# Optimization experiments

Measured on AMD Instinct MI355X. Metric: run time of the kernel, lower is better.

Reference implementation:

```python
import jax, jax.numpy as jnp
import numpy as np

EPS = 1e-8  # torch cosine_similarity default eps


def setup_inputs() -> dict:
    key = jax.random.key(0)
    x = jax.random.normal(key, (256, 200, 1024), dtype=jnp.float32)
    return {"x": x}


def reference(x):
    # x: [B, c, l]
    # Cosine-similarity Gram matrix, fused: dot(i,j) / max(||x_i||*||x_j||, eps)
    norms = jnp.linalg.norm(x, axis=-1)                      # [B, c]
    dots = jnp.einsum('bil,bjl->bij', x, x)                  # [B, c, c]
    sim = dots / jnp.maximum(norms[:, :, None] * norms[:, None, :], EPS)
    atten = jax.nn.softmax(sim, axis=-1)                     # [B, c, c]
    out = jnp.einsum('bij,bjl->bil', atten, x) + x           # bmm + residual
    return out
```

## Files before the change

kernel.cpp:

```cpp
#include <hip/hip_runtime.h>
#include <math.h>


typedef unsigned int uint32;
typedef __attribute__((ext_vector_type(8))) short bf16x8;
typedef __attribute__((ext_vector_type(4))) float f32x4;

#define CC 200
#define LL 1024
#define EPSV 1e-8f
#define PLSTR 116
#define XASTR 36
#define XBSTR 132

__device__ __forceinline__ uint32 bfb(float f) {
  uint32 u = __float_as_uint(f);
  u += 0x7fffu + ((u >> 16) & 1u);
  return u >> 16;
}

__global__ __launch_bounds__(512, 1)
void spe_attn_kernel(const float* __restrict__ x, float* __restrict__ out) {
  const int tid  = threadIdx.x;
  const int lane = tid & 63;
  const int w    = tid >> 6;
  const int lm   = lane & 15;
  const int lg   = lane >> 4;
  const int bidx = blockIdx.x;
  const float* xb = x + (size_t)bidx * (CC * LL);
  float* ob       = out + (size_t)bidx * (CC * LL);

  __shared__ uint32 LDS[39312];
  uint32* pl    = LDS;
  uint32* xa0   = LDS + 24128;
  uint32* xa1   = LDS + 31616;
  uint32* xbuf  = LDS + 24128;
  float*  norms = (float*)(LDS + 39104);

  const bool two = (w < 5);
  const int rb0 = w;
  const int rb1 = two ? (w + 8) : w;

  const f32x4 fz = {0.f, 0.f, 0.f, 0.f};
  f32x4 acc[2][13];
  #pragma unroll
  for (int i = 0; i < 2; ++i)
    #pragma unroll
    for (int j = 0; j < 13; ++j) acc[i][j] = fz;

  if (tid < 288) { xa0[7200 + tid] = 0u; xa1[7200 + tid] = 0u; }

  float4 vst[7];
  #pragma unroll
  for (int i = 0; i < 7; ++i) {
    int idx = tid + i * 512;
    if (idx < 3200) {
      int row = idx >> 4, c4 = idx & 15;
      vst[i] = *(const float4*)(xb + row * LL + c4 * 4);
    }
  }
  #pragma unroll
  for (int i = 0; i < 7; ++i) {
    int idx = tid + i * 512;
    if (idx < 3200) {
      int row = idx >> 4, c4 = idx & 15;
      uint2 wv;
      wv.x = bfb(vst[i].x) | (bfb(vst[i].y) << 16);
      wv.y = bfb(vst[i].z) | (bfb(vst[i].w) << 16);
      *(uint2*)&xa0[row * XASTR + c4 * 2] = wv;
    }
  }

  for (int s = 0; s < 16; ++s) {
    __syncthreads();
    if (s + 1 < 16) {
      #pragma unroll
      for (int i = 0; i < 7; ++i) {
        int idx = tid + i * 512;
        if (idx < 3200) {
          int row = idx >> 4, c4 = idx & 15;
          vst[i] = *(const float4*)(xb + row * LL + (s + 1) * 64 + c4 * 4);
        }
      }
    }
    const uint32* cur = (s & 1) ? xa1 : xa0;
    #pragma unroll
    for (int ks = 0; ks < 2; ++ks) {
      bf16x8 a0 = *(const bf16x8*)&cur[(rb0 * 16 + lm) * XASTR + ks * 16 + lg * 4];
      bf16x8 a1 = a0;
      if (two) a1 = *(const bf16x8*)&cur[(rb1 * 16 + lm) * XASTR + ks * 16 + lg * 4];
      #pragma unroll
      for (int ct = 0; ct < 13; ++ct) {
        bf16x8 bf = *(const bf16x8*)&cur[(ct * 16 + lm) * XASTR + ks * 16 + lg * 4];
        acc[0][ct] = __builtin_amdgcn_mfma_f32_16x16x32_bf16(a0, bf, acc[0][ct], 0, 0, 0);
        if (two)
          acc[1][ct] = __builtin_amdgcn_mfma_f32_16x16x32_bf16(a1, bf, acc[1][ct], 0, 0, 0);
      }
    }
    if (s + 1 < 16) {
      uint32* nxt = (s & 1) ? xa0 : xa1;
      #pragma unroll
      for (int i = 0; i < 7; ++i) {
        int idx = tid + i * 512;
        if (idx < 3200) {
          int row = idx >> 4, c4 = idx & 15;
          uint2 wv;
          wv.x = bfb(vst[i].x) | (bfb(vst[i].y) << 16);
          wv.y = bfb(vst[i].z) | (bfb(vst[i].w) << 16);
          *(uint2*)&nxt[row * XASTR + c4 * 2] = wv;
        }
      }
    }
  }

  #pragma unroll
  for (int rbi = 0; rbi < 2; ++rbi) {
    if (rbi == 0 || two) {
      int rb = rbi ? rb1 : rb0;
      #pragma unroll
      for (int ct = 0; ct < 13; ++ct) {
        if (ct == rb) {
          #pragma unroll
          for (int r = 0; r < 4; ++r) {
            int ri = lg * 4 + r;
            if (lm == ri) norms[rb * 16 + ri] = sqrtf(acc[rbi][ct][r]);
          }
        }
      }
    }
  }
  __syncthreads();

  float cn[13];
  #pragma unroll
  for (int ct = 0; ct < 13; ++ct) cn[ct] = norms[ct * 16 + lm];

  #pragma unroll
  for (int rbi = 0; rbi < 2; ++rbi) {
    if (rbi == 0 || two) {
      int rb = rbi ? rb1 : rb0;
      #pragma unroll
      for (int r = 0; r < 4; ++r) {
        int grow = rb * 16 + lg * 4 + r;
        float rn = norms[grow];
        float sv[13];
        float m = -INFINITY;
        #pragma unroll
        for (int ct = 0; ct < 13; ++ct) {
          int gc = ct * 16 + lm;
          float sval = acc[rbi][ct][r] / fmaxf(rn * cn[ct], EPSV);
          sval = (gc < CC) ? sval : -INFINITY;
          sv[ct] = sval;
          m = fmaxf(m, sval);
        }
        #pragma unroll
        for (int off = 1; off < 16; off <<= 1) m = fmaxf(m, __shfl_xor(m, off));
        float sum = 0.f;
        #pragma unroll
        for (int ct = 0; ct < 13; ++ct) {
          float e = __expf(sv[ct] - m);
          sv[ct] = e;
          sum += e;
        }
        #pragma unroll
        for (int off = 1; off < 16; off <<= 1) sum += __shfl_xor(sum, off);
        float inv = 1.0f / sum;
        #pragma unroll
        for (int ct = 0; ct < 13; ++ct) {
          int gc = ct * 16 + lm;
          float p = sv[ct] * inv + ((gc == grow) ? 1.0f : 0.0f);
          uint32 pb = bfb(p);
          uint32 qb = (uint32)__shfl_xor((int)pb, 1);
          if (!(lane & 1)) pl[grow * PLSTR + ct * 8 + (lm >> 1)] = pb | (qb << 16);
        }
      }
      for (int i = lane; i < 256; i += 64) {
        int rr = i >> 4, c = i & 15;
        if (c < 12) pl[(rb * 16 + rr) * PLSTR + 100 + c] = 0u;
      }
    }
  }

  bf16x8 pa[2][7];
  #pragma unroll
  for (int ks = 0; ks < 7; ++ks) {
    pa[0][ks] = *(const bf16x8*)&pl[(rb0 * 16 + lm) * PLSTR + ks * 16 + lg * 4];
    if (two)
      pa[1][ks] = *(const bf16x8*)&pl[(rb1 * 16 + lm) * PLSTR + ks * 16 + lg * 4];
  }

  float pva[14], pvb[14];
  #pragma unroll
  for (int p = 0; p < 14; ++p) {
    int kp = p * 8 + w;
    int r0 = kp * 2, r1 = r0 + 1;
    pva[p] = (r0 < CC) ? xb[r0 * LL + lane] : 0.f;
    pvb[p] = (r1 < CC) ? xb[r1 * LL + lane] : 0.f;
  }

  for (int nc = 0; nc < 16; ++nc) {
    const int n0 = nc * 64;
    __syncthreads();
    #pragma unroll
    for (int p = 0; p < 14; ++p) {
      int kp = p * 8 + w;
      xbuf[lane * XBSTR + kp] = bfb(pva[p]) | (bfb(pvb[p]) << 16);
    }
    __syncthreads();
    if (nc + 1 < 16) {
      const int n1 = (nc + 1) * 64;
      #pragma unroll
      for (int p = 0; p < 14; ++p) {
        int kp = p * 8 + w;
        int r0 = kp * 2, r1 = r0 + 1;
        pva[p] = (r0 < CC) ? xb[r0 * LL + n1 + lane] : 0.f;
        pvb[p] = (r1 < CC) ? xb[r1 * LL + n1 + lane] : 0.f;
      }
    }

    f32x4 acc2[2][4];
    #pragma unroll
    for (int i = 0; i < 2; ++i)
      #pragma unroll
      for (int j = 0; j < 4; ++j) acc2[i][j] = fz;

    #pragma unroll
    for (int ks = 0; ks < 7; ++ks) {
      #pragma unroll
      for (int ct = 0; ct < 4; ++ct) {
        bf16x8 b = *(const bf16x8*)&xbuf[(ct * 16 + lm) * XBSTR + ks * 16 + lg * 4];
        acc2[0][ct] = __builtin_amdgcn_mfma_f32_16x16x32_bf16(pa[0][ks], b, acc2[0][ct], 0, 0, 0);
        if (two)
          acc2[1][ct] = __builtin_amdgcn_mfma_f32_16x16x32_bf16(pa[1][ks], b, acc2[1][ct], 0, 0, 0);
      }
    }

    #pragma unroll
    for (int rbi = 0; rbi < 2; ++rbi) {
      if (rbi == 0 || two) {
        int rb = rbi ? rb1 : rb0;
        #pragma unroll
        for (int ct = 0; ct < 4; ++ct) {
          #pragma unroll
          for (int r = 0; r < 4; ++r) {
            int grow = rb * 16 + lg * 4 + r;
            if (grow < CC) ob[grow * LL + n0 + ct * 16 + lm] = acc2[rbi][ct][r];
          }
        }
      }
    }
  }
}

extern "C" void kernel_launch(void* const* d_in, const int* in_sizes, int n_in,
                              void* d_out, int out_size, void* d_ws, size_t ws_size,
                              hipStream_t stream) {
  const float* x = (const float*)d_in[0];
  float* out = (float*)d_out;
  const int B = in_sizes[0] / (CC * LL);
  spe_attn_kernel<<<dim3(B), dim3(512), 0, stream>>>(x, out);
}
```

Baseline: 157.5 us.

## Split fused attention into gram/softmax and PV kernels with two blocks per batch

Replaces the single fused kernel (one block per batch, occupancy 1) with two kernels, each launched with 2*B blocks. The first computes half the Gram row tiles plus diagonal norms and writes softmax probabilities to workspace. The second computes P·X over half the columns, with an XOR swizzle on the LDS layout to reduce bank conflicts. The aim is more parallelism and higher occupancy through smaller LDS per block, at the cost of computing the Gram matrix twice per batch, re-reading x, an extra launch, and a workspace round trip. The fused kernel is kept as a fallback when the workspace is too small.

Measured after the change: 331.5 us. 2.1x slower.

```diff
diff --git a/kernel.cpp b/kernel.cpp
--- a/kernel.cpp
+++ b/kernel.cpp
@@ -9,8 +9,8 @@
 #define CC 200
 #define LL 1024
 #define EPSV 1e-8f
-#define PLSTR 116
 #define XASTR 36
+#define PWS 112
 #define XBSTR 132
 
 __device__ __forceinline__ uint32 bfb(float f) {
@@ -19,8 +19,268 @@
   return u >> 16;
 }
 
+__global__ __launch_bounds__(512, 4)
+void gram_sm_kernel(const float* __restrict__ x, uint32* __restrict__ pws) {
+  const int tid  = threadIdx.x;
+  const int lane = tid & 63;
+  const int w    = tid >> 6;
+  const int lm   = lane & 15;
+  const int lg   = lane >> 4;
+  const int nb   = gridDim.x >> 1;
+  const int bid  = blockIdx.x;
+  const int half = (bid >= nb) ? 1 : 0;
+  const int batch = bid - half * nb;
+  const float* xb = x + (size_t)batch * (CC * LL);
+  uint32* pgl     = pws + (size_t)batch * (208 * PWS);
+
+  const int hb     = half ? 7 : 0;
+  const int ntiles = half ? 6 : 7;
+  const int dbase  = half ? 0 : 7;
+  const int ndiag  = 13 - ntiles;
+
+  __shared__ uint32 LDS[15184];
+  uint32* xa0   = LDS;
+  uint32* xa1   = LDS + 7488;
+  float*  norms = (float*)(LDS + 14976);
+
+  const f32x4 fz = {0.f, 0.f, 0.f, 0.f};
+  f32x4 acc[13];
+  #pragma unroll
+  for (int j = 0; j < 13; ++j) acc[j] = fz;
+
+  if (tid < 288) { xa0[7200 + tid] = 0u; xa1[7200 + tid] = 0u; }
+
+  float4 vst[7];
+  #pragma unroll
+  for (int i = 0; i < 7; ++i) {
+    int idx = tid + i * 512;
+    if (idx < 3200) {
+      int row = idx >> 4, c4 = idx & 15;
+      vst[i] = *(const float4*)(xb + row * LL + c4 * 4);
+    }
+  }
+  #pragma unroll
+  for (int i = 0; i < 7; ++i) {
+    int idx = tid + i * 512;
+    if (idx < 3200) {
+      int row = idx >> 4, c4 = idx & 15;
+      uint2 wv;
+      wv.x = bfb(vst[i].x) | (bfb(vst[i].y) << 16);
+      wv.y = bfb(vst[i].z) | (bfb(vst[i].w) << 16);
+      *(uint2*)&xa0[row * XASTR + c4 * 2] = wv;
+    }
+  }
+
+  for (int s = 0; s < 16; ++s) {
+    __syncthreads();
+    if (s + 1 < 16) {
+      #pragma unroll
+      for (int i = 0; i < 7; ++i) {
+        int idx = tid + i * 512;
+        if (idx < 3200) {
+          int row = idx >> 4, c4 = idx & 15;
+          vst[i] = *(const float4*)(xb + row * LL + (s + 1) * 64 + c4 * 4);
+        }
+      }
+    }
+    const uint32* cur = (s & 1) ? xa1 : xa0;
+    #pragma unroll
+    for (int ks = 0; ks < 2; ++ks) {
+      if (w < ntiles) {
+        bf16x8 a = *(const bf16x8*)&cur[((hb + w) * 16 + lm) * XASTR + ks * 16 + lg * 4];
+        #pragma unroll
+        for (int ct = 0; ct < 13; ++ct) {
+          bf16x8 b = *(const bf16x8*)&cur[(ct * 16 + lm) * XASTR + ks * 16 + lg * 4];
+          acc[ct] = __builtin_amdgcn_mfma_f32_16x16x32_bf16(a, b, acc[ct], 0, 0, 0);
+        }
+      } else if (w == ntiles) {
+        #pragma unroll
+        for (int d = 0; d < 7; ++d) {
+          if (d < ndiag) {
+            bf16x8 f = *(const bf16x8*)&cur[((dbase + d) * 16 + lm) * XASTR + ks * 16 + lg * 4];
+            acc[d] = __builtin_amdgcn_mfma_f32_16x16x32_bf16(f, f, acc[d], 0, 0, 0);
+          }
+        }
+      }
+    }
+    if (s + 1 < 16) {
+      uint32* nxt = (s & 1) ? xa0 : xa1;
+      #pragma unroll
+      for (int i = 0; i < 7; ++i) {
+        int idx = tid + i * 512;
+        if (idx < 3200) {
+          int row = idx >> 4, c4 = idx & 15;
+          uint2 wv;
+          wv.x = bfb(vst[i].x) | (bfb(vst[i].y) << 16);
+          wv.y = bfb(vst[i].z) | (bfb(vst[i].w) << 16);
+          *(uint2*)&nxt[row * XASTR + c4 * 2] = wv;
+        }
+      }
+    }
+  }
+
+  if (w < ntiles) {
+    const int t = hb + w;
+    #pragma unroll
+    for (int ct = 0; ct < 13; ++ct) {
+      if (ct == t) {
+        #pragma unroll
+        for (int r = 0; r < 4; ++r) {
+          int ri = lg * 4 + r;
+          if (lm == ri) norms[t * 16 + ri] = sqrtf(acc[ct][r]);
+        }
+      }
+    }
+  } else if (w == ntiles) {
+    #pragma unroll
+    for (int d = 0; d < 7; ++d) {
+      if (d < ndiag) {
+        int t = dbase + d;
+        #pragma unroll
+        for (int r = 0; r < 4; ++r) {
+          int ri = lg * 4 + r;
+          if (lm == ri) norms[t * 16 + ri] = sqrtf(acc[d][r]);
+        }
+      }
+    }
+  }
+  __syncthreads();
+
+  if (w < ntiles) {
+    const int t = hb + w;
+    float cn[13];
+    #pragma unroll
+    for (int ct = 0; ct < 13; ++ct) cn[ct] = norms[ct * 16 + lm];
+
+    #pragma unroll
+    for (int r = 0; r < 4; ++r) {
+      int grow = t * 16 + lg * 4 + r;
+      float rn = norms[grow];
+      float sv[13];
+      float m = -INFINITY;
+      #pragma unroll
+      for (int ct = 0; ct < 13; ++ct) {
+        int gc = ct * 16 + lm;
+        float sval = acc[ct][r] / fmaxf(rn * cn[ct], EPSV);
+        sval = (gc < CC) ? sval : -INFINITY;
+        sv[ct] = sval;
+        m = fmaxf(m, sval);
+      }
+      #pragma unroll
+      for (int off = 1; off < 16; off <<= 1) m = fmaxf(m, __shfl_xor(m, off));
+      float sum = 0.f;
+      #pragma unroll
+      for (int ct = 0; ct < 13; ++ct) {
+        float e = __expf(sv[ct] - m);
+        sv[ct] = e;
+        sum += e;
+      }
+      #pragma unroll
+      for (int off = 1; off < 16; off <<= 1) sum += __shfl_xor(sum, off);
+      float inv = 1.0f / sum;
+      #pragma unroll
+      for (int ct = 0; ct < 13; ++ct) {
+        int gc = ct * 16 + lm;
+        float p = sv[ct] * inv + ((gc == grow) ? 1.0f : 0.0f);
+        uint32 pb16 = bfb(p);
+        uint32 qb = (uint32)__shfl_xor((int)pb16, 1);
+        if (!(lane & 1)) pgl[grow * PWS + ct * 8 + (lm >> 1)] = pb16 | (qb << 16);
+      }
+    }
+    #pragma unroll
+    for (int i = 0; i < 3; ++i) {
+      int idx = lane + i * 64;
+      int rr = idx & 15, c = idx >> 4;
+      pgl[(t * 16 + rr) * PWS + 100 + c] = 0u;
+    }
+  }
+}
+
+__global__ __launch_bounds__(512, 4)
+void pv_kernel(const float* __restrict__ x, const uint32* __restrict__ pws,
+               float* __restrict__ out) {
+  const int tid  = threadIdx.x;
+  const int lane = tid & 63;
+  const int w    = tid >> 6;
+  const int lm   = lane & 15;
+  const int lg   = lane >> 4;
+  const int nb   = gridDim.x >> 1;
+  const int bid  = blockIdx.x;
+  const int half = (bid >= nb) ? 1 : 0;
+  const int batch = bid - half * nb;
+  const float* xb = x + (size_t)batch * (CC * LL);
+  float* ob       = out + (size_t)batch * (CC * LL);
+  const uint32* pgl = pws + (size_t)batch * (208 * PWS);
+
+  const bool two = (w < 5);
+  const int rb0 = w;
+  const int rb1 = two ? (w + 8) : w;
+
+  __shared__ uint32 xbuf[8448];
+
+  bf16x8 pa[2][7];
+  #pragma unroll
+  for (int ks = 0; ks < 7; ++ks) {
+    pa[0][ks] = *(const bf16x8*)&pgl[(rb0 * 16 + lm) * PWS + ks * 16 + lg * 4];
+    if (two)
+      pa[1][ks] = *(const bf16x8*)&pgl[(rb1 * 16 + lm) * PWS + ks * 16 + lg * 4];
+  }
+
+  const f32x4 fz = {0.f, 0.f, 0.f, 0.f};
+  for (int nc = 0; nc < 8; ++nc) {
+    const int n0 = half * 512 + nc * 64;
+    __syncthreads();
+    #pragma unroll
+    for (int p = 0; p < 14; ++p) {
+      int kp = p * 8 + w;
+      int r0 = kp * 2, r1 = r0 + 1;
+      float va = (r0 < CC) ? xb[r0 * LL + n0 + lane] : 0.f;
+      float vb = (r1 < CC) ? xb[r1 * LL + n0 + lane] : 0.f;
+      int sk = kp ^ (((lane >> 3) & 7) << 2);
+      xbuf[lane * XBSTR + sk] = bfb(va) | (bfb(vb) << 16);
+    }
+    __syncthreads();
+
+    f32x4 acc2[2][4];
+    #pragma unroll
+    for (int i = 0; i < 2; ++i)
+      #pragma unroll
+      for (int j = 0; j < 4; ++j) acc2[i][j] = fz;
+
+    #pragma unroll
+    for (int ks = 0; ks < 7; ++ks) {
+      #pragma unroll
+      for (int ct = 0; ct < 4; ++ct) {
+        int col = ct * 16 + lm;
+        int kpb = ks * 16 + lg * 4;
+        int skb = kpb ^ (((col >> 3) & 7) << 2);
+        bf16x8 b = *(const bf16x8*)&xbuf[col * XBSTR + skb];
+        acc2[0][ct] = __builtin_amdgcn_mfma_f32_16x16x32_bf16(pa[0][ks], b, acc2[0][ct], 0, 0, 0);
+        if (two)
+          acc2[1][ct] = __builtin_amdgcn_mfma_f32_16x16x32_bf16(pa[1][ks], b, acc2[1][ct], 0, 0, 0);
+      }
+    }
+
+    #pragma unroll
+    for (int rbi = 0; rbi < 2; ++rbi) {
+      if (rbi == 0 || two) {
+        int rb = rbi ? rb1 : rb0;
+        #pragma unroll
+        for (int ct = 0; ct < 4; ++ct) {
+          #pragma unroll
+          for (int r = 0; r < 4; ++r) {
+            int grow = rb * 16 + lg * 4 + r;
+            if (grow < CC) ob[grow * LL + n0 + ct * 16 + lm] = acc2[rbi][ct][r];
+          }
+        }
+      }
+    }
+  }
+}
+
+#define PLSTR 116
 __global__ __launch_bounds__(512, 1)
-void spe_attn_kernel(const float* __restrict__ x, float* __restrict__ out) {
+void spe_attn_fused(const float* __restrict__ x, float* __restrict__ out) {
   const int tid  = threadIdx.x;
   const int lane = tid & 63;
   const int w    = tid >> 6;
@@ -34,7 +294,7 @@
   uint32* pl    = LDS;
   uint32* xa0   = LDS + 24128;
   uint32* xa1   = LDS + 31616;
-  uint32* xbuf  = LDS + 24128;
+  uint32* xbufl = LDS + 24128;
   float*  norms = (float*)(LDS + 39104);
 
   const bool two = (w < 5);
@@ -204,7 +464,7 @@
     #pragma unroll
     for (int p = 0; p < 14; ++p) {
       int kp = p * 8 + w;
-      xbuf[lane * XBSTR + kp] = bfb(pva[p]) | (bfb(pvb[p]) << 16);
+      xbufl[lane * XBSTR + kp] = bfb(pva[p]) | (bfb(pvb[p]) << 16);
     }
     __syncthreads();
     if (nc + 1 < 16) {
@@ -228,7 +488,7 @@
     for (int ks = 0; ks < 7; ++ks) {
       #pragma unroll
       for (int ct = 0; ct < 4; ++ct) {
-        bf16x8 b = *(const bf16x8*)&xbuf[(ct * 16 + lm) * XBSTR + ks * 16 + lg * 4];
+        bf16x8 b = *(const bf16x8*)&xbufl[(ct * 16 + lm) * XBSTR + ks * 16 + lg * 4];
         acc2[0][ct] = __builtin_amdgcn_mfma_f32_16x16x32_bf16(pa[0][ks], b, acc2[0][ct], 0, 0, 0);
         if (two)
           acc2[1][ct] = __builtin_amdgcn_mfma_f32_16x16x32_bf16(pa[1][ks], b, acc2[1][ct], 0, 0, 0);
@@ -258,5 +518,11 @@
   const float* x = (const float*)d_in[0];
   float* out = (float*)d_out;
   const int B = in_sizes[0] / (CC * LL);
-  spe_attn_kernel<<<dim3(B), dim3(512), 0, stream>>>(x, out);
+  const size_t need = (size_t)B * 208 * PWS * 4;
+  if (ws_size >= need) {
+    gram_sm_kernel<<<dim3(2 * B), dim3(512), 0, stream>>>(x, (uint32*)d_ws);
+    pv_kernel<<<dim3(2 * B), dim3(512), 0, stream>>>(x, (const uint32*)d_ws, out);
+  } else {
+    spe_attn_fused<<<dim3(B), dim3(512), 0, stream>>>(x, out);
+  }
 }
```

## Double-buffer transposed x tiles in PV phase, drop a barrier, add setprio

Applied to the files above, without the earlier changes.

The second GEMM phase now writes the bf16 transposed x tile into two alternating LDS buffers. The next tile's global loads are issued before the MFMA loop and written to the other buffer afterward, which removes one __syncthreads per chunk. Each thread loads four consecutive rows and writes them as one uint2 with a narrower stride. s_setprio raises wave priority around both MFMA loops. The cost is extra LDS footprint reusing the xa region and different bank-conflict behaviour from the new stride.

Measured after the change: 151.0 us. -4.1%, faster.

```diff
diff --git a/kernel.cpp b/kernel.cpp
--- a/kernel.cpp
+++ b/kernel.cpp
@@ -11,7 +11,7 @@
 #define EPSV 1e-8f
 #define PLSTR 116
 #define XASTR 36
-#define XBSTR 132
+#define TSTR 116
 
 __device__ __forceinline__ uint32 bfb(float f) {
   uint32 u = __float_as_uint(f);
@@ -34,7 +34,8 @@
   uint32* pl    = LDS;
   uint32* xa0   = LDS + 24128;
   uint32* xa1   = LDS + 31616;
-  uint32* xbuf  = LDS + 24128;
+  uint32* xbf0  = LDS + 24128;
+  uint32* xbf1  = LDS + 31616;
   float*  norms = (float*)(LDS + 39104);
 
   const bool two = (w < 5);
@@ -84,6 +85,7 @@
       }
     }
     const uint32* cur = (s & 1) ? xa1 : xa0;
+    __builtin_amdgcn_s_setprio(1);
     #pragma unroll
     for (int ks = 0; ks < 2; ++ks) {
       bf16x8 a0 = *(const bf16x8*)&cur[(rb0 * 16 + lm) * XASTR + ks * 16 + lg * 4];
@@ -97,6 +99,7 @@
           acc[1][ct] = __builtin_amdgcn_mfma_f32_16x16x32_bf16(a1, bf, acc[1][ct], 0, 0, 0);
       }
     }
+    __builtin_amdgcn_s_setprio(0);
     if (s + 1 < 16) {
       uint32* nxt = (s & 1) ? xa0 : xa1;
       #pragma unroll
@@ -189,49 +192,70 @@
       pa[1][ks] = *(const bf16x8*)&pl[(rb1 * 16 + lm) * PLSTR + ks * 16 + lg * 4];
   }
 
-  float pva[14], pvb[14];
-  #pragma unroll
-  for (int p = 0; p < 14; ++p) {
-    int kp = p * 8 + w;
-    int r0 = kp * 2, r1 = r0 + 1;
-    pva[p] = (r0 < CC) ? xb[r0 * LL + lane] : 0.f;
-    pvb[p] = (r1 < CC) ? xb[r1 * LL + lane] : 0.f;
+  float pv[7][4];
+  #pragma unroll
+  for (int p = 0; p < 7; ++p) {
+    int rb4 = (p * 8 + w) * 4;
+    #pragma unroll
+    for (int q = 0; q < 4; ++q) {
+      int r = rb4 + q;
+      pv[p][q] = (r < CC) ? xb[r * LL + lane] : 0.f;
+    }
+  }
+  #pragma unroll
+  for (int p = 0; p < 7; ++p) {
+    int kpp = p * 8 + w;
+    uint2 wv;
+    wv.x = bfb(pv[p][0]) | (bfb(pv[p][1]) << 16);
+    wv.y = bfb(pv[p][2]) | (bfb(pv[p][3]) << 16);
+    *(uint2*)&xbf0[lane * TSTR + 2 * kpp] = wv;
   }
 
   for (int nc = 0; nc < 16; ++nc) {
     const int n0 = nc * 64;
     __syncthreads();
-    #pragma unroll
-    for (int p = 0; p < 14; ++p) {
-      int kp = p * 8 + w;
-      xbuf[lane * XBSTR + kp] = bfb(pva[p]) | (bfb(pvb[p]) << 16);
-    }
-    __syncthreads();
     if (nc + 1 < 16) {
-      const int n1 = (nc + 1) * 64;
-      #pragma unroll
-      for (int p = 0; p < 14; ++p) {
-        int kp = p * 8 + w;
-        int r0 = kp * 2, r1 = r0 + 1;
-        pva[p] = (r0 < CC) ? xb[r0 * LL + n1 + lane] : 0.f;
-        pvb[p] = (r1 < CC) ? xb[r1 * LL + n1 + lane] : 0.f;
-      }
-    }
-
+      const int n1 = n0 + 64;
+      #pragma unroll
+      for (int p = 0; p < 7; ++p) {
+        int rb4 = (p * 8 + w) * 4;
+        #pragma unroll
+        for (int q = 0; q < 4; ++q) {
+          int r = rb4 + q;
+          pv[p][q] = (r < CC) ? xb[r * LL + n1 + lane] : 0.f;
+        }
+      }
+    }
+
+    const uint32* XC = (nc & 1) ? xbf1 : xbf0;
     f32x4 acc2[2][4];
     #pragma unroll
     for (int i = 0; i < 2; ++i)
       #pragma unroll
       for (int j = 0; j < 4; ++j) acc2[i][j] = fz;
 
+    __builtin_amdgcn_s_setprio(1);
     #pragma unroll
     for (int ks = 0; ks < 7; ++ks) {
       #pragma unroll
       for (int ct = 0; ct < 4; ++ct) {
-        bf16x8 b = *(const bf16x8*)&xbuf[(ct * 16 + lm) * XBSTR + ks * 16 + lg * 4];
+        bf16x8 b = *(const bf16x8*)&XC[(ct * 16 + lm) * TSTR + ks * 16 + lg * 4];
         acc2[0][ct] = __builtin_amdgcn_mfma_f32_16x16x32_bf16(pa[0][ks], b, acc2[0][ct], 0, 0, 0);
         if (two)
           acc2[1][ct] = __builtin_amdgcn_mfma_f32_16x16x32_bf16(pa[1][ks], b, acc2[1][ct], 0, 0, 0);
+      }
+    }
+    __builtin_amdgcn_s_setprio(0);
+
+    if (nc + 1 < 16) {
+      uint32* XN = (nc & 1) ? xbf0 : xbf1;
+      #pragma unroll
+      for (int p = 0; p < 7; ++p) {
+        int kpp = p * 8 + w;
+        uint2 wv;
+        wv.x = bfb(pv[p][0]) | (bfb(pv[p][1]) << 16);
+        wv.y = bfb(pv[p][2]) | (bfb(pv[p][3]) << 16);
+        *(uint2*)&XN[lane * TSTR + 2 * kpp] = wv;
       }
     }
 
```
